# Performance work log

Measured on AMD Instinct MI355X. Metric: run time of the kernel, lower is better.

The kernel has to match this reference:

```python
import jax, jax.numpy as jnp
import numpy as np
from math import sqrt

B, S, E, H = 2, 2048, 1024, 16

def setup_inputs() -> dict:
    key = jax.random.key(0)
    k1, k2, k3, k4, k5 = jax.random.split(key, 5)
    bound_in = 1.0 / sqrt(E)
    return {
        "inputs": jax.random.normal(k1, (B, S, E), dtype=jnp.float32),
        "W_in": jax.random.uniform(k2, (3 * E, E), dtype=jnp.float32, minval=-bound_in, maxval=bound_in),
        "b_in": jax.random.uniform(k3, (3 * E,), dtype=jnp.float32, minval=-bound_in, maxval=bound_in),
        "W_out": jax.random.uniform(k4, (E, E), dtype=jnp.float32, minval=-bound_in, maxval=bound_in),
        "b_out": jax.random.uniform(k5, (E,), dtype=jnp.float32, minval=-bound_in, maxval=bound_in),
    }

def reference(inputs, W_in, b_in, W_out, b_out):
    # Eval-mode forward (dropout is identity when not training).
    b, s, e = inputs.shape
    hd = e // H
    qkv = jnp.einsum('bse,fe->bsf', inputs, W_in) + b_in  # [B,S,3E]
    q, k, v = jnp.split(qkv, 3, axis=-1)
    # [B,S,E] -> [B,H,S,hd]
    to_heads = lambda t: t.reshape(b, s, H, hd).transpose(0, 2, 1, 3)
    q, k, v = to_heads(q), to_heads(k), to_heads(v)
    scores = jnp.einsum('bhqd,bhkd->bhqk', q, k) / jnp.sqrt(jnp.float32(hd))
    causal = jnp.tril(jnp.ones((s, s), dtype=bool))
    scores = jnp.where(causal, scores, -jnp.inf)
    attn = jax.nn.softmax(scores, axis=-1)  # stable max-subtract softmax, same math
    out = jnp.einsum('bhqk,bhkd->bhqd', attn, v)  # [B,H,S,hd]
    out = out.transpose(0, 2, 1, 3).reshape(b, s, e)
    return jnp.einsum('bse,fe->bsf', out, W_out) + b_out
```

## Files before the change

kernel.cpp:

```cpp
#include <hip/hip_runtime.h>
#include <hip/hip_bf16.h>
#include <stdint.h>

#define SS 2048
#define EE 1024
#define HH 16
#define HD 64

#define QSCALE 0.1803368801111137f

typedef __attribute__((ext_vector_type(8))) short short8;
typedef __attribute__((ext_vector_type(4))) float f32x4;

__device__ __forceinline__ short f2bf(float f) {
  union { float f; uint32_t u; } x; x.f = f;
  uint32_t r = x.u + 0x7fffu + ((x.u >> 16) & 1u);
  return (short)(r >> 16);
}

__device__ __forceinline__ uint32_t pk_bf16(float a, float b) {
#if __has_builtin(__builtin_amdgcn_cvt_pk_bf16_f32)
  typedef __attribute__((ext_vector_type(2))) __bf16 bf16x2_t;
  union { bf16x2_t v; uint32_t u; } x;
  x.v = __builtin_amdgcn_cvt_pk_bf16_f32(a, b);
  return x.u;
#else
  return (uint32_t)(uint16_t)f2bf(a) | ((uint32_t)(uint16_t)f2bf(b) << 16);
#endif
}

__device__ __forceinline__ void async_cp16(const void* g, void* l) {
  __builtin_amdgcn_global_load_lds((const __attribute__((address_space(1))) void*)g,
                                   (__attribute__((address_space(3))) void*)l, 16, 0, 0);
}

#define N4_X  1048576
#define N4_W1 786432
#define N4_W2 262144
__global__ __launch_bounds__(256) void cvt_all(
    const float* __restrict__ x, const float* __restrict__ w1,
    const float* __restrict__ w2,
    short* __restrict__ xb, short* __restrict__ w1b, short* __restrict__ w2b)
{
  int i = blockIdx.x * 256 + threadIdx.x;
  const float* src; short* dst; int off;
  if (i < N4_X)            { src = x;  dst = xb;  off = i; }
  else if (i < N4_X+N4_W1) { src = w1; dst = w1b; off = i - N4_X; }
  else                     { src = w2; dst = w2b; off = i - N4_X - N4_W1; }
  float4 v = *(const float4*)&src[(size_t)off * 4];
  uint2 pk;
  pk.x = pk_bf16(v.x, v.y);
  pk.y = pk_bf16(v.z, v.w);
  *(uint2*)&dst[(size_t)off * 4] = pk;
}

template<int MODE>
__global__ __launch_bounds__(256) void gemm_lds(
    const short* __restrict__ A, const short* __restrict__ Bw,
    const float* __restrict__ bias,
    float* __restrict__ C,
    short* __restrict__ qw, short* __restrict__ kw, short* __restrict__ vw,
    int M, int N, int K)
{
  __shared__ short smem[(MODE == 1) ? 17408 : 8192];
  short* sA = smem;
  short* sB = smem + 4096;
  const int tid = threadIdx.x;
  const int lane = tid & 63;
  const int wv = tid >> 6;
  const int wm = (wv >> 1) * 64;
  const int wn = (wv & 1) * 64;
  const int t = lane >> 4;
  const int lr = lane & 15;
  const int bm = blockIdx.y * 128;
  const int bn = blockIdx.x * 128;

  f32x4 acc[4][4];
  #pragma unroll
  for (int i = 0; i < 4; ++i)
    #pragma unroll
    for (int j = 0; j < 4; ++j) acc[i][j] = (f32x4){0.f, 0.f, 0.f, 0.f};

  for (int k0 = 0; k0 < K; k0 += 32) {
    __syncthreads();
    #pragma unroll
    for (int it = 0; it < 2; ++it) {
      int c = it * 256 + wv * 64 + lane;
      int row = c >> 2;
      int ch = (c & 3) * 8;
      async_cp16(&A[(size_t)(bm + row) * K + k0 + ch],
                 (char*)sA + (size_t)(it * 256 + wv * 64) * 16);
      async_cp16(&Bw[(size_t)(bn + row) * K + k0 + ch],
                 (char*)sB + (size_t)(it * 256 + wv * 64) * 16);
    }
    __syncthreads();
    short8 af[4], bfr[4];
    #pragma unroll
    for (int i = 0; i < 4; ++i) af[i] = *(const short8*)&sA[(wm + i*16 + lr)*32 + t*8];
    #pragma unroll
    for (int j = 0; j < 4; ++j) bfr[j] = *(const short8*)&sB[(wn + j*16 + lr)*32 + t*8];
    #pragma unroll
    for (int i = 0; i < 4; ++i)
      #pragma unroll
      for (int j = 0; j < 4; ++j)
        acc[i][j] = __builtin_amdgcn_mfma_f32_16x16x32_bf16(af[i], bfr[j], acc[i][j], 0, 0, 0);
  }

  if (MODE == 1 && bn >= 2048) {
    __syncthreads();
    short* vx = smem;
    #pragma unroll
    for (int i = 0; i < 4; ++i) {
      int row0 = wm + i*16 + t*4;
      #pragma unroll
      for (int j = 0; j < 4; ++j) {
        int cl = wn + j*16 + lr;
        float bv = bias[bn + cl];
        #pragma unroll
        for (int r = 0; r < 4; ++r)
          vx[cl*136 + row0 + r] = f2bf(acc[i][j][r] + bv);
      }
    }
    __syncthreads();
    int h0 = (bn - 2048) >> 6;
    int b_ = bm >> 11;
    int s0 = bm & 2047;
    #pragma unroll
    for (int it = 0; it < 8; ++it) {
      int cc = it * 256 + tid;
      int cl = cc >> 4;
      int ck = cc & 15;
      int h = h0 + (cl >> 6);
      int d = cl & 63;
      *(uint4*)&vw[((size_t)(b_*HH + h)*HD + d)*SS + s0 + ck*8] =
          *(const uint4*)&vx[cl*136 + ck*8];
    }
    return;
  }

  #pragma unroll
  for (int i = 0; i < 4; ++i) {
    int row0 = bm + wm + i*16 + t*4;
    #pragma unroll
    for (int j = 0; j < 4; ++j) {
      int col = bn + wn + j*16 + lr;
      float bv = bias[col];
      #pragma unroll
      for (int r = 0; r < 4; ++r) {
        float v = acc[i][j][r] + bv;
        int rr = row0 + r;
        if (MODE == 0) {
          C[(size_t)rr * N + col] = v;
        } else {
          int e = col & 1023;
          int h = e >> 6, d = e & 63;
          int b_ = rr >> 11, s = rr & 2047;
          if (col < 1024)
            qw[((size_t)(b_*HH + h)*SS + s)*HD + d] = f2bf(v * QSCALE);
          else
            kw[((size_t)(b_*HH + h)*SS + s)*HD + d] = f2bf(v);
        }
      }
    }
  }
}

template<int MODE, typename TA>
__global__ __launch_bounds__(256) void gemm_bt(
    const TA* __restrict__ A, const float* __restrict__ Bw,
    const float* __restrict__ bias,
    float* __restrict__ C,
    short* __restrict__ qw, short* __restrict__ kw, short* __restrict__ vw,
    int M, int N, int K)
{
  __shared__ short sA[128*32];
  __shared__ short sB[128*32];
  const int tid = threadIdx.x;
  const int lane = tid & 63;
  const int wv = tid >> 6;
  const int wm = (wv >> 1) * 64;
  const int wn = (wv & 1) * 64;
  const int t = lane >> 4;
  const int lr = lane & 15;
  const int bm = blockIdx.y * 128;
  const int bn = blockIdx.x * 128;

  f32x4 acc[4][4];
  #pragma unroll
  for (int i = 0; i < 4; ++i)
    #pragma unroll
    for (int j = 0; j < 4; ++j) acc[i][j] = (f32x4){0.f, 0.f, 0.f, 0.f};

  for (int k0 = 0; k0 < K; k0 += 32) {
    __syncthreads();
    if constexpr (sizeof(TA) == 4) {
      #pragma unroll
      for (int it = 0; it < 4; ++it) {
        int c = it * 256 + tid;
        int row = c >> 3, ch = (c & 7) * 4;
        float4 va = *(const float4*)&A[(size_t)(bm + row)*K + k0 + ch];
        uint2 pk; pk.x = pk_bf16(va.x, va.y); pk.y = pk_bf16(va.z, va.w);
        *(uint2*)&sA[row*32 + ch] = pk;
      }
    } else {
      #pragma unroll
      for (int it = 0; it < 2; ++it) {
        int c = it * 256 + tid;
        int row = c >> 2, ch = (c & 3) * 8;
        *(uint4*)&sA[row*32 + ch] = *(const uint4*)&A[(size_t)(bm + row)*K + k0 + ch];
      }
    }
    #pragma unroll
    for (int it = 0; it < 4; ++it) {
      int c = it * 256 + tid;
      int row = c >> 3, ch = (c & 7) * 4;
      float4 vb = *(const float4*)&Bw[(size_t)(bn + row)*K + k0 + ch];
      uint2 pk; pk.x = pk_bf16(vb.x, vb.y); pk.y = pk_bf16(vb.z, vb.w);
      *(uint2*)&sB[row*32 + ch] = pk;
    }
    __syncthreads();
    short8 af[4], bfr[4];
    #pragma unroll
    for (int i = 0; i < 4; ++i) af[i] = *(const short8*)&sA[(wm + i*16 + lr)*32 + t*8];
    #pragma unroll
    for (int j = 0; j < 4; ++j) bfr[j] = *(const short8*)&sB[(wn + j*16 + lr)*32 + t*8];
    #pragma unroll
    for (int i = 0; i < 4; ++i)
      #pragma unroll
      for (int j = 0; j < 4; ++j)
        acc[i][j] = __builtin_amdgcn_mfma_f32_16x16x32_bf16(af[i], bfr[j], acc[i][j], 0, 0, 0);
  }

  #pragma unroll
  for (int i = 0; i < 4; ++i) {
    int row0 = bm + wm + i*16 + t*4;
    #pragma unroll
    for (int j = 0; j < 4; ++j) {
      int col = bn + wn + j*16 + lr;
      float bv = bias[col];
      #pragma unroll
      for (int r = 0; r < 4; ++r) {
        float v = acc[i][j][r] + bv;
        int rr = row0 + r;
        if (MODE == 0) {
          C[(size_t)rr * N + col] = v;
        } else {
          int which = col >> 10;
          int e = col & 1023;
          int h = e >> 6, d = e & 63;
          int b_ = rr >> 11, s = rr & 2047;
          if (which == 0)
            qw[((size_t)(b_*HH + h)*SS + s)*HD + d] = f2bf(v * QSCALE);
          else if (which == 1)
            kw[((size_t)(b_*HH + h)*SS + s)*HD + d] = f2bf(v);
          else
            vw[((size_t)(b_*HH + h)*HD + d)*SS + s] = f2bf(v);
        }
      }
    }
  }
}

__global__ __launch_bounds__(512) void attn_kernel(
    const short* __restrict__ Q, const short* __restrict__ K,
    const short* __restrict__ Vt, short* __restrict__ O)
{
  __shared__ short sK[2][128*64];
  __shared__ short sV[2][64*128];
  __shared__ short sP[8][16*128];
  const int tid = threadIdx.x;
  const int lane = tid & 63;
  const int w = tid >> 6;
  const int t = lane >> 4;
  const int lr = lane & 15;
  const int pairIdx = blockIdx.x >> 5;
  const int bh = blockIdx.x & 31;
  const int b = bh >> 4, h = bh & 15;
  const short* Qb = Q  + (size_t)bh * SS * HD;
  const short* Kb = K  + (size_t)bh * SS * HD;
  const short* Vb = Vt + (size_t)bh * HD * SS;
  short* sPw = sP[w];

  auto stage = [&](int buf, int kb) {
    #pragma unroll
    for (int it2 = 0; it2 < 2; ++it2) {
      int s = it2 * 512 + tid;
      int krow = s >> 3;
      int kcc = (s & 7) ^ (krow & 7);
      async_cp16(&Kb[(size_t)(kb + krow) * HD + kcc * 8],
                 (char*)sK[buf] + (size_t)(it2 * 512 + w * 64) * 16);
      int d = s >> 4;
      int vcc = (s & 15) ^ (d & 15);
      async_cp16(&Vb[(size_t)d * SS + kb + vcc * 8],
                 (char*)sV[buf] + (size_t)(it2 * 512 + w * 64) * 16);
    }
  };

  #pragma unroll 1
  for (int phase = 0; phase < 2; ++phase) {
    const int qt = phase ? (15 - pairIdx) : pairIdx;
    const int qrow0 = qt * 128 + w * 16;
    const int niter = qt + 1;

    short8 qf[2];
    #pragma unroll
    for (int st = 0; st < 2; ++st)
      qf[st] = *(const short8*)&Qb[(size_t)(qrow0 + lr) * HD + st*32 + t*8];

    f32x4 o[4];
    #pragma unroll
    for (int jd = 0; jd < 4; ++jd) o[jd] = (f32x4){0.f, 0.f, 0.f, 0.f};
    float m = -1e30f, l = 0.f;

    stage(0, 0);
    __syncthreads();
    int cur = 0;

    #pragma unroll 1
    for (int it = 0; it < niter; ++it) {
      const int kb = it * 128;
      if (it + 1 < niter) stage(cur ^ 1, kb + 128);

      const short* sKc = sK[cur];
      const short* sVc = sV[cur];

      f32x4 sc[8];
      #pragma unroll
      for (int c = 0; c < 8; ++c) sc[c] = (f32x4){0.f,0.f,0.f,0.f};
      #pragma unroll
      for (int c = 0; c < 8; ++c) {
        int krow = c*16 + lr;
        #pragma unroll
        for (int st = 0; st < 2; ++st) {
          int slot = krow*8 + ((st*4 + t) ^ (krow & 7));
          short8 kf = *(const short8*)&sKc[slot*8];
          sc[c] = __builtin_amdgcn_mfma_f32_16x16x32_bf16(kf, qf[st], sc[c], 0, 0, 0);
        }
      }

      if (it == niter - 1) {
        int qg = qrow0 + lr;
        #pragma unroll
        for (int c = 0; c < 8; ++c)
          #pragma unroll
          for (int r = 0; r < 4; ++r)
            if (kb + c*16 + t*4 + r > qg) sc[c][r] = -1e30f;
      }

      float mx = sc[0][0];
      #pragma unroll
      for (int c = 0; c < 8; ++c)
        #pragma unroll
        for (int r = 0; r < 4; ++r) mx = fmaxf(mx, sc[c][r]);
      mx = fmaxf(mx, __shfl_xor(mx, 16));
      mx = fmaxf(mx, __shfl_xor(mx, 32));

      float mn = fmaxf(m, mx);
      float alpha = exp2f(m - mn);
      m = mn;
      float rs = 0.f;
      #pragma unroll
      for (int c = 0; c < 8; ++c)
        #pragma unroll
        for (int r = 0; r < 4; ++r) {
          sc[c][r] = exp2f(sc[c][r] - mn);
          rs += sc[c][r];
        }
      rs += __shfl_xor(rs, 16);
      rs += __shfl_xor(rs, 32);
      l = l * alpha + rs;

      float alr[4];
      #pragma unroll
      for (int r = 0; r < 4; ++r) alr[r] = __shfl(alpha, 20*t + r);
      #pragma unroll
      for (int jd = 0; jd < 4; ++jd)
        #pragma unroll
        for (int r = 0; r < 4; ++r) o[jd][r] *= alr[r];

      #pragma unroll
      for (int c = 0; c < 8; ++c) {
        uint2 pk2;
        pk2.x = pk_bf16(sc[c][0], sc[c][1]);
        pk2.y = pk_bf16(sc[c][2], sc[c][3]);
        int chunk = 2*c + (t >> 1);
        int slot = lr*16 + (chunk ^ lr);
        *(uint2*)&sPw[slot*8 + (t & 1)*4] = pk2;
      }
      #pragma unroll
      for (int f = 0; f < 4; ++f) {
        int pslot = lr*16 + ((f*4 + t) ^ lr);
        short8 pf = *(const short8*)&sPw[pslot*8];
        #pragma unroll
        for (int jd = 0; jd < 4; ++jd) {
          int d = jd*16 + lr;
          int vslot = d*16 + ((f*4 + t) ^ (d & 15));
          short8 vf = *(const short8*)&sVc[vslot*8];
          o[jd] = __builtin_amdgcn_mfma_f32_16x16x32_bf16(pf, vf, o[jd], 0, 0, 0);
        }
      }

      __syncthreads();
      cur ^= 1;
    }

    float linv[4];
    #pragma unroll
    for (int r = 0; r < 4; ++r) linv[r] = 1.0f / __shfl(l, 20*t + r);
    #pragma unroll
    for (int jd = 0; jd < 4; ++jd)
      #pragma unroll
      for (int r = 0; r < 4; ++r) {
        int qrow = qrow0 + t*4 + r;
        int d = jd*16 + lr;
        O[((size_t)(b * SS + qrow)) * EE + h * HD + d] = f2bf(o[jd][r] * linv[r]);
      }
  }
}

extern "C" void kernel_launch(void* const* d_in, const int* in_sizes, int n_in,
                              void* d_out, int out_size, void* d_ws, size_t ws_size,
                              hipStream_t stream) {
  const float* X     = (const float*)d_in[0];
  const float* W_in  = (const float*)d_in[1];
  const float* b_in  = (const float*)d_in[2];
  const float* W_out = (const float*)d_in[3];
  const float* b_out = (const float*)d_in[4];
  float* out = (float*)d_out;

  char* ws = (char*)d_ws;
  const size_t MB = 1024 * 1024;
  const int M = 2 * SS;

  if (ws_size >= 48 * MB) {
    short* Xb   = (short*)(ws);
    short* Wb1  = (short*)(ws + 8  * MB);
    short* Wb2  = (short*)(ws + 14 * MB);
    short* q_ws = (short*)(ws + 16 * MB);
    short* k_ws = (short*)(ws + 24 * MB);
    short* v_ws = (short*)(ws + 32 * MB);
    short* attn = (short*)(ws + 40 * MB);

    cvt_all<<<8192, 256, 0, stream>>>(X, W_in, W_out, Xb, Wb1, Wb2);
    gemm_lds<1><<<dim3(24, 32), 256, 0, stream>>>(
        Xb, Wb1, b_in, nullptr, q_ws, k_ws, v_ws, M, 3 * EE, EE);
    attn_kernel<<<dim3(256), 512, 0, stream>>>(q_ws, k_ws, v_ws, attn);
    gemm_lds<0><<<dim3(8, 32), 256, 0, stream>>>(
        attn, Wb2, b_out, out, nullptr, nullptr, nullptr, M, EE, EE);
  } else {
    short* q_ws = (short*)(ws);
    short* k_ws = (short*)(ws + 8  * MB);
    short* v_ws = (short*)(ws + 16 * MB);
    short* attn = (short*)(ws + 24 * MB);

    gemm_bt<1, float><<<dim3(24, 32), 256, 0, stream>>>(
        X, W_in, b_in, nullptr, q_ws, k_ws, v_ws, M, 3 * EE, EE);
    attn_kernel<<<dim3(256), 512, 0, stream>>>(q_ws, k_ws, v_ws, attn);
    gemm_bt<0, short><<<dim3(8, 32), 256, 0, stream>>>(
        attn, W_out, b_out, out, nullptr, nullptr, nullptr, M, EE, EE);
  }
}
```

Baseline: 208.3 us.

## Drop bf16 pre-conversion pass; fuse fp32 loads into register-prefetched GEMM

Removes the separate kernel that converted X, W_in and W_out to bf16. The GEMMs now read fp32 straight from global memory and convert to bf16 while storing into LDS. The main loop prefetches the next K-slice into registers while the current one is computed, replacing the async global-to-LDS copies. This saves one launch and a round trip through bf16 copies, but each GEMM now reads twice the bytes for fp32 operands and uses more registers, which may lower occupancy.

New measurement: 238.5 us. 14.5% more time.

```diff
diff --git a/kernel.cpp b/kernel.cpp
--- a/kernel.cpp
+++ b/kernel.cpp
@@ -34,29 +34,9 @@
                                    (__attribute__((address_space(3))) void*)l, 16, 0, 0);
 }
 
-#define N4_X  1048576
-#define N4_W1 786432
-#define N4_W2 262144
-__global__ __launch_bounds__(256) void cvt_all(
-    const float* __restrict__ x, const float* __restrict__ w1,
-    const float* __restrict__ w2,
-    short* __restrict__ xb, short* __restrict__ w1b, short* __restrict__ w2b)
-{
-  int i = blockIdx.x * 256 + threadIdx.x;
-  const float* src; short* dst; int off;
-  if (i < N4_X)            { src = x;  dst = xb;  off = i; }
-  else if (i < N4_X+N4_W1) { src = w1; dst = w1b; off = i - N4_X; }
-  else                     { src = w2; dst = w2b; off = i - N4_X - N4_W1; }
-  float4 v = *(const float4*)&src[(size_t)off * 4];
-  uint2 pk;
-  pk.x = pk_bf16(v.x, v.y);
-  pk.y = pk_bf16(v.z, v.w);
-  *(uint2*)&dst[(size_t)off * 4] = pk;
-}
-
-template<int MODE>
-__global__ __launch_bounds__(256) void gemm_lds(
-    const short* __restrict__ A, const short* __restrict__ Bw,
+template<int MODE, typename TA, typename TB>
+__global__ __launch_bounds__(256) void gemm_pipe(
+    const TA* __restrict__ A, const TB* __restrict__ Bw,
     const float* __restrict__ bias,
     float* __restrict__ C,
     short* __restrict__ qw, short* __restrict__ kw, short* __restrict__ vw,
@@ -81,17 +61,82 @@
     #pragma unroll
     for (int j = 0; j < 4; ++j) acc[i][j] = (f32x4){0.f, 0.f, 0.f, 0.f};
 
+  float4 fa_c[4], fa_n[4], fb_c[4], fb_n[4];
+  uint4  ua_c[2], ua_n[2], ub_c[2], ub_n[2];
+
+  auto loadA = [&](int k0, float4* f4, uint4* u4) {
+    if constexpr (sizeof(TA) == 4) {
+      #pragma unroll
+      for (int it = 0; it < 4; ++it) {
+        int c = it * 256 + tid; int row = c >> 3, ch = (c & 7) * 4;
+        f4[it] = *(const float4*)&A[(size_t)(bm + row) * K + k0 + ch];
+      }
+    } else {
+      #pragma unroll
+      for (int it = 0; it < 2; ++it) {
+        int c = it * 256 + tid; int row = c >> 2, ch = (c & 3) * 8;
+        u4[it] = *(const uint4*)&A[(size_t)(bm + row) * K + k0 + ch];
+      }
+    }
+  };
+  auto loadB = [&](int k0, float4* f4, uint4* u4) {
+    if constexpr (sizeof(TB) == 4) {
+      #pragma unroll
+      for (int it = 0; it < 4; ++it) {
+        int c = it * 256 + tid; int row = c >> 3, ch = (c & 7) * 4;
+        f4[it] = *(const float4*)&Bw[(size_t)(bn + row) * K + k0 + ch];
+      }
+    } else {
+      #pragma unroll
+      for (int it = 0; it < 2; ++it) {
+        int c = it * 256 + tid; int row = c >> 2, ch = (c & 3) * 8;
+        u4[it] = *(const uint4*)&Bw[(size_t)(bn + row) * K + k0 + ch];
+      }
+    }
+  };
+  auto writeA = [&](const float4* f4, const uint4* u4) {
+    if constexpr (sizeof(TA) == 4) {
+      #pragma unroll
+      for (int it = 0; it < 4; ++it) {
+        int c = it * 256 + tid; int row = c >> 3, ch = (c & 7) * 4;
+        uint2 pk; pk.x = pk_bf16(f4[it].x, f4[it].y); pk.y = pk_bf16(f4[it].z, f4[it].w);
+        *(uint2*)&sA[row*32 + ch] = pk;
+      }
+    } else {
+      #pragma unroll
+      for (int it = 0; it < 2; ++it) {
+        int c = it * 256 + tid; int row = c >> 2, ch = (c & 3) * 8;
+        *(uint4*)&sA[row*32 + ch] = u4[it];
+      }
+    }
+  };
+  auto writeB = [&](const float4* f4, const uint4* u4) {
+    if constexpr (sizeof(TB) == 4) {
+      #pragma unroll
+      for (int it = 0; it < 4; ++it) {
+        int c = it * 256 + tid; int row = c >> 3, ch = (c & 7) * 4;
+        uint2 pk; pk.x = pk_bf16(f4[it].x, f4[it].y); pk.y = pk_bf16(f4[it].z, f4[it].w);
+        *(uint2*)&sB[row*32 + ch] = pk;
+      }
+    } else {
+      #pragma unroll
+      for (int it = 0; it < 2; ++it) {
+        int c = it * 256 + tid; int row = c >> 2, ch = (c & 3) * 8;
+        *(uint4*)&sB[row*32 + ch] = u4[it];
+      }
+    }
+  };
+
+  loadA(0, fa_c, ua_c);
+  loadB(0, fb_c, ub_c);
+
   for (int k0 = 0; k0 < K; k0 += 32) {
     __syncthreads();
-    #pragma unroll
-    for (int it = 0; it < 2; ++it) {
-      int c = it * 256 + wv * 64 + lane;
-      int row = c >> 2;
-      int ch = (c & 3) * 8;
-      async_cp16(&A[(size_t)(bm + row) * K + k0 + ch],
-                 (char*)sA + (size_t)(it * 256 + wv * 64) * 16);
-      async_cp16(&Bw[(size_t)(bn + row) * K + k0 + ch],
-                 (char*)sB + (size_t)(it * 256 + wv * 64) * 16);
+    writeA(fa_c, ua_c);
+    writeB(fb_c, ub_c);
+    if (k0 + 32 < K) {
+      loadA(k0 + 32, fa_n, ua_n);
+      loadB(k0 + 32, fb_n, ub_n);
     }
     __syncthreads();
     short8 af[4], bfr[4];
@@ -104,6 +149,10 @@
       #pragma unroll
       for (int j = 0; j < 4; ++j)
         acc[i][j] = __builtin_amdgcn_mfma_f32_16x16x32_bf16(af[i], bfr[j], acc[i][j], 0, 0, 0);
+    #pragma unroll
+    for (int it = 0; it < 4; ++it) { fa_c[it] = fa_n[it]; fb_c[it] = fb_n[it]; }
+    #pragma unroll
+    for (int it = 0; it < 2; ++it) { ua_c[it] = ua_n[it]; ub_c[it] = ub_n[it]; }
   }
 
   if (MODE == 1 && bn >= 2048) {
@@ -159,102 +208,6 @@
             qw[((size_t)(b_*HH + h)*SS + s)*HD + d] = f2bf(v * QSCALE);
           else
             kw[((size_t)(b_*HH + h)*SS + s)*HD + d] = f2bf(v);
-        }
-      }
-    }
-  }
-}
-
-template<int MODE, typename TA>
-__global__ __launch_bounds__(256) void gemm_bt(
-    const TA* __restrict__ A, const float* __restrict__ Bw,
-    const float* __restrict__ bias,
-    float* __restrict__ C,
-    short* __restrict__ qw, short* __restrict__ kw, short* __restrict__ vw,
-    int M, int N, int K)
-{
-  __shared__ short sA[128*32];
-  __shared__ short sB[128*32];
-  const int tid = threadIdx.x;
-  const int lane = tid & 63;
-  const int wv = tid >> 6;
-  const int wm = (wv >> 1) * 64;
-  const int wn = (wv & 1) * 64;
-  const int t = lane >> 4;
-  const int lr = lane & 15;
-  const int bm = blockIdx.y * 128;
-  const int bn = blockIdx.x * 128;
-
-  f32x4 acc[4][4];
-  #pragma unroll
-  for (int i = 0; i < 4; ++i)
-    #pragma unroll
-    for (int j = 0; j < 4; ++j) acc[i][j] = (f32x4){0.f, 0.f, 0.f, 0.f};
-
-  for (int k0 = 0; k0 < K; k0 += 32) {
-    __syncthreads();
-    if constexpr (sizeof(TA) == 4) {
-      #pragma unroll
-      for (int it = 0; it < 4; ++it) {
-        int c = it * 256 + tid;
-        int row = c >> 3, ch = (c & 7) * 4;
-        float4 va = *(const float4*)&A[(size_t)(bm + row)*K + k0 + ch];
-        uint2 pk; pk.x = pk_bf16(va.x, va.y); pk.y = pk_bf16(va.z, va.w);
-        *(uint2*)&sA[row*32 + ch] = pk;
-      }
-    } else {
-      #pragma unroll
-      for (int it = 0; it < 2; ++it) {
-        int c = it * 256 + tid;
-        int row = c >> 2, ch = (c & 3) * 8;
-        *(uint4*)&sA[row*32 + ch] = *(const uint4*)&A[(size_t)(bm + row)*K + k0 + ch];
-      }
-    }
-    #pragma unroll
-    for (int it = 0; it < 4; ++it) {
-      int c = it * 256 + tid;
-      int row = c >> 3, ch = (c & 7) * 4;
-      float4 vb = *(const float4*)&Bw[(size_t)(bn + row)*K + k0 + ch];
-      uint2 pk; pk.x = pk_bf16(vb.x, vb.y); pk.y = pk_bf16(vb.z, vb.w);
-      *(uint2*)&sB[row*32 + ch] = pk;
-    }
-    __syncthreads();
-    short8 af[4], bfr[4];
-    #pragma unroll
-    for (int i = 0; i < 4; ++i) af[i] = *(const short8*)&sA[(wm + i*16 + lr)*32 + t*8];
-    #pragma unroll
-    for (int j = 0; j < 4; ++j) bfr[j] = *(const short8*)&sB[(wn + j*16 + lr)*32 + t*8];
-    #pragma unroll
-    for (int i = 0; i < 4; ++i)
-      #pragma unroll
-      for (int j = 0; j < 4; ++j)
-        acc[i][j] = __builtin_amdgcn_mfma_f32_16x16x32_bf16(af[i], bfr[j], acc[i][j], 0, 0, 0);
-  }
-
-  #pragma unroll
-  for (int i = 0; i < 4; ++i) {
-    int row0 = bm + wm + i*16 + t*4;
-    #pragma unroll
-    for (int j = 0; j < 4; ++j) {
-      int col = bn + wn + j*16 + lr;
-      float bv = bias[col];
-      #pragma unroll
-      for (int r = 0; r < 4; ++r) {
-        float v = acc[i][j][r] + bv;
-        int rr = row0 + r;
-        if (MODE == 0) {
-          C[(size_t)rr * N + col] = v;
-        } else {
-          int which = col >> 10;
-          int e = col & 1023;
-          int h = e >> 6, d = e & 63;
-          int b_ = rr >> 11, s = rr & 2047;
-          if (which == 0)
-            qw[((size_t)(b_*HH + h)*SS + s)*HD + d] = f2bf(v * QSCALE);
-          else if (which == 1)
-            kw[((size_t)(b_*HH + h)*SS + s)*HD + d] = f2bf(v);
-          else
-            vw[((size_t)(b_*HH + h)*HD + d)*SS + s] = f2bf(v);
         }
       }
     }
@@ -430,33 +383,18 @@
 
   char* ws = (char*)d_ws;
   const size_t MB = 1024 * 1024;
+  short* q_ws = (short*)(ws);
+  short* k_ws = (short*)(ws + 8  * MB);
+  short* v_ws = (short*)(ws + 16 * MB);
+  short* attn = (short*)(ws + 24 * MB);
+
   const int M = 2 * SS;
 
-  if (ws_size >= 48 * MB) {
-    short* Xb   = (short*)(ws);
-    short* Wb1  = (short*)(ws + 8  * MB);
-    short* Wb2  = (short*)(ws + 14 * MB);
-    short* q_ws = (short*)(ws + 16 * MB);
-    short* k_ws = (short*)(ws + 24 * MB);
-    short* v_ws = (short*)(ws + 32 * MB);
-    short* attn = (short*)(ws + 40 * MB);
-
-    cvt_all<<<8192, 256, 0, stream>>>(X, W_in, W_out, Xb, Wb1, Wb2);
-    gemm_lds<1><<<dim3(24, 32), 256, 0, stream>>>(
-        Xb, Wb1, b_in, nullptr, q_ws, k_ws, v_ws, M, 3 * EE, EE);
-    attn_kernel<<<dim3(256), 512, 0, stream>>>(q_ws, k_ws, v_ws, attn);
-    gemm_lds<0><<<dim3(8, 32), 256, 0, stream>>>(
-        attn, Wb2, b_out, out, nullptr, nullptr, nullptr, M, EE, EE);
-  } else {
-    short* q_ws = (short*)(ws);
-    short* k_ws = (short*)(ws + 8  * MB);
-    short* v_ws = (short*)(ws + 16 * MB);
-    short* attn = (short*)(ws + 24 * MB);
-
-    gemm_bt<1, float><<<dim3(24, 32), 256, 0, stream>>>(
-        X, W_in, b_in, nullptr, q_ws, k_ws, v_ws, M, 3 * EE, EE);
-    attn_kernel<<<dim3(256), 512, 0, stream>>>(q_ws, k_ws, v_ws, attn);
-    gemm_bt<0, short><<<dim3(8, 32), 256, 0, stream>>>(
-        attn, W_out, b_out, out, nullptr, nullptr, nullptr, M, EE, EE);
-  }
-}
+  gemm_pipe<1, float, float><<<dim3(24, 32), 256, 0, stream>>>(
+      X, W_in, b_in, nullptr, q_ws, k_ws, v_ws, M, 3 * EE, EE);
+
+  attn_kernel<<<dim3(256), 512, 0, stream>>>(q_ws, k_ws, v_ws, attn);
+
+  gemm_pipe<0, short, float><<<dim3(8, 32), 256, 0, stream>>>(
+      attn, W_out, b_out, out, nullptr, nullptr, nullptr, M, EE, EE);
+}
```
